# Performance work log

Measured on AMD Instinct MI355X. Metric: run time of the kernel, lower is better.

The kernel has to match this reference:

```python
import jax, jax.numpy as jnp
import numpy as np

V, B, C, H, W, D = 3, 2, 16, 128, 128, 32


def _skew(w):
    wx, wy, wz = w[..., 0], w[..., 1], w[..., 2]
    z = jnp.zeros_like(wx)
    return jnp.stack([
        jnp.stack([z, -wz, wy], -1),
        jnp.stack([wz, z, -wx], -1),
        jnp.stack([-wy, wx, z], -1)], -2)


def _rodrigues(w):
    th = jnp.linalg.norm(w, axis=-1, keepdims=True)
    n = w / (th + 1e-8)
    K = _skew(n)
    th = th[..., None]
    I = jnp.eye(3, dtype=w.dtype)
    return I + jnp.sin(th) * K + (1.0 - jnp.cos(th)) * (K @ K)


def setup_inputs() -> dict:
    key = jax.random.key(0)
    k1, k2, k3, k4 = jax.random.split(key, 4)
    features = jax.random.normal(k1, (V, B, C, H, W), jnp.float32)
    Kmat = jnp.array([[1.2 * W, 0.0, W / 2.0], [0.0, 1.2 * W, H / 2.0], [0.0, 0.0, 1.0]], jnp.float32)
    intrinsics = jnp.tile(Kmat, (V, B, 1, 1))
    rotvec = 0.05 * jax.random.normal(k2, (V, B, 3), jnp.float32)
    R = _rodrigues(rotvec)                                  # (V,B,3,3)
    t = 0.1 * jax.random.normal(k3, (V, B, 3), jnp.float32)
    top = jnp.concatenate([R, t[..., None]], -1)            # (V,B,3,4)
    bot = jnp.broadcast_to(jnp.array([0.0, 0.0, 0.0, 1.0], jnp.float32), (V, B, 1, 4))
    cam_to_world = jnp.concatenate([top, bot], -2)          # (V,B,4,4)
    depth_hypo = 1.0 + 9.0 * jax.random.uniform(k4, (B, D, H, W), jnp.float32)
    return {"features": features, "intrinsics": intrinsics,
            "cam_to_world": cam_to_world, "depth_hypo": depth_hypo}


def _grid_sample(img, grid):
    # img (B,C,H,W), grid (B,Hg,Wg,2) in [-1,1]; bilinear, zeros padding, align_corners=False
    Bb, Cc, Hh, Ww = img.shape
    gx = (grid[..., 0] + 1.0) * (Ww * 0.5) - 0.5
    gy = (grid[..., 1] + 1.0) * (Hh * 0.5) - 0.5
    x0f, y0f = jnp.floor(gx), jnp.floor(gy)
    fx, fy = gx - x0f, gy - y0f
    x0, y0 = x0f.astype(jnp.int32), y0f.astype(jnp.int32)

    def gather(xi, yi):
        valid = ((xi >= 0) & (xi < Ww) & (yi >= 0) & (yi < Hh)).astype(img.dtype)
        xc = jnp.clip(xi, 0, Ww - 1)
        yc = jnp.clip(yi, 0, Hh - 1)
        v = jax.vmap(lambda im, y, x: im[:, y, x])(img, yc, xc)  # (B,C,Hg,Wg)
        return v * valid[:, None]

    v00 = gather(x0, y0)
    v01 = gather(x0 + 1, y0)
    v10 = gather(x0, y0 + 1)
    v11 = gather(x0 + 1, y0 + 1)
    fx_, fy_ = fx[:, None], fy[:, None]
    return (v00 * (1 - fx_) * (1 - fy_) + v01 * fx_ * (1 - fy_)
            + v10 * (1 - fx_) * fy_ + v11 * fx_ * fy_)


def _unfold5(x):
    # x (B,K,H,W) -> (B,K,25,H,W); kernel 5, stride 1, pad 2; row-major kernel order (torch F.unfold)
    Hh, Ww = x.shape[-2], x.shape[-1]
    xp = jnp.pad(x, ((0, 0), (0, 0), (2, 2), (2, 2)))
    return jnp.stack([xp[..., i:i + Hh, j:j + Ww] for i in range(5) for j in range(5)], axis=2)


def _safe_norm(x, axis, keepdims=False):
    s = jnp.sum(x * x, axis=axis, keepdims=keepdims)
    z = s == 0
    return jnp.where(z, 0.0, jnp.sqrt(jnp.where(z, 1.0, s)))


def _homo_warp(src_f, depth_hypo, src_K, src_c2w, ref_K, ref_c2w):
    Bb, Cc, Hh, Ww = src_f.shape
    Dd = depth_hypo.shape[1]
    src_w2c = jnp.linalg.inv(src_c2w)
    ref_w2c = jnp.linalg.inv(ref_c2w)
    src_KK = src_w2c.at[:, :3, :3].set(src_K)
    ref_KK = ref_w2c.at[:, :3, :3].set(ref_K)
    proj = (src_KK @ src_w2c) @ jnp.linalg.inv(ref_KK @ ref_w2c)
    rot, trans = proj[:, :3, :3], proj[:, :3, 3:4]
    # NOTE: source uses arange(height) for both axes (square images assumed)
    ys, xs = jnp.meshgrid(jnp.arange(Hh, dtype=jnp.float32), jnp.arange(Hh, dtype=jnp.float32), indexing='ij')
    xyz = jnp.stack([xs.ravel(), ys.ravel(), jnp.ones(Hh * Ww, jnp.float32)], 0)  # (3,HW)
    rot_xyz = jnp.einsum('bij,jn->bin', rot, xyz)                                 # (B,3,HW)
    pts = rot_xyz[:, :, None, :] * depth_hypo.reshape(Bb, 1, Dd, -1) + trans[:, :, None, :]
    xy = pts[:, :2] / pts[:, 2:3]
    gx = xy[:, 0] / ((Ww - 1) / 2.0) - 1.0
    gy = xy[:, 1] / ((Hh - 1) / 2.0) - 1.0
    grid = jax.lax.stop_gradient(jnp.stack([gx, gy], -1).reshape(Bb, Dd * Hh, Ww, 2))
    return _grid_sample(src_f, grid).reshape(Bb, Cc, Dd, Hh, Ww)


def reference(features, intrinsics, cam_to_world, depth_hypo):
    Vv = features.shape[0]
    ref_f = features[0]
    warped = jnp.stack([
        _homo_warp(features[i], depth_hypo, intrinsics[i], cam_to_world[i],
                   intrinsics[0], cam_to_world[0]) for i in range(1, Vv)], 0)
    # faithful to in-place ref_volume.sub_: view k compares against ref - cumsum(warped[:k+1])
    diff = ref_f[None, :, :, None] - jnp.cumsum(warped, 0)        # (V-1,B,C,D,H,W)
    costs = _safe_norm(diff, axis=2)                              # (V-1,B,D,H,W)
    cost_volume = jnp.min(costs, axis=0)                          # (B,D,H,W)

    cnb = _unfold5(cost_volume)                                   # (B,D,25,H,W)
    dnb = _unfold5(depth_hypo)                                    # (B,D,25,H,W)
    w_depth = jax.nn.softmax(jnp.abs(dnb - dnb[:, :, 12:13]), axis=2)
    fnb = _unfold5(ref_f)                                         # (B,C,25,H,W)
    w_feat = _safe_norm(fnb - fnb[:, :, 12:13], axis=1, keepdims=True)  # (B,1,25,H,W)
    agg = jnp.sum(cnb * (w_depth * w_feat), axis=2)               # (B,D,H,W)

    prob = jax.nn.softmax(agg, axis=1)
    return jnp.sum(prob * depth_hypo, axis=1)                     # (B,H,W)
```

## Files before the change

kernel.cpp:

```cpp
#include <hip/hip_runtime.h>
#include <hip/hip_fp16.h>
#include <math.h>

#define Vn 3
#define Bn 2
#define Cn 16
#define Hn 128
#define Wn 128
#define Dn 32
#define HWn (Hn*Wn)
#define KD 4
#define PX 8

__device__ __forceinline__ void loadC8(float* r, const __half* p) {
    union { float4 f; __half2 h[4]; } u;
    u.f = *(const float4*)p;
    #pragma unroll
    for (int j = 0; j < 4; j++) {
        float2 a = __half22float2(u.h[j]);
        r[2*j] = a.x; r[2*j+1] = a.y;
    }
}

__global__ void transpose_kernel(const float* __restrict__ feat,
                                 __half* __restrict__ featH,
                                 const float* __restrict__ intr,
                                 const float* __restrict__ c2w,
                                 float* __restrict__ proj) {
    int idx = blockIdx.x * blockDim.x + threadIdx.x;
    if (idx < Vn * Bn * HWn) {
        int p  = idx % HWn;
        int vb = idx / HWn;
        const float* src = feat + (size_t)vb * Cn * HWn + p;
        union { float4 f[2]; __half h[16]; } u;
        #pragma unroll
        for (int c = 0; c < Cn; c++) u.h[c] = __float2half(src[(size_t)c * HWn]);
        float4* dst = (float4*)(featH + (size_t)idx * Cn);
        dst[0] = u.f[0];
        dst[1] = u.f[1];
    }

    if (blockIdx.x == 0 && threadIdx.x < (Vn - 1) * Bn) {
        int t  = threadIdx.x;
        int vi = t / Bn;
        int b  = t % Bn;
        int v  = vi + 1;

        const float* Ks = intr + (v * Bn + b) * 9;
        const float* Cs = c2w  + (v * Bn + b) * 16;
        const float* Kr = intr + (0 * Bn + b) * 9;
        const float* Cr = c2w  + (0 * Bn + b) * 16;

        float Ms[9], ms[3], Mr[9], mr[3];
        for (int which = 0; which < 2; which++) {
            const float* K = which ? Kr : Ks;
            const float* C = which ? Cr : Cs;
            float* M  = which ? Mr : Ms;
            float* mv = which ? mr : ms;
            float R[9], tt[3];
            for (int i = 0; i < 3; i++) {
                for (int j = 0; j < 3; j++) R[i*3+j] = C[i*4+j];
                tt[i] = C[i*4+3];
            }
            float tw[3];
            for (int i = 0; i < 3; i++)
                tw[i] = -(R[0*3+i]*tt[0] + R[1*3+i]*tt[1] + R[2*3+i]*tt[2]);
            for (int i = 0; i < 3; i++)
                for (int j = 0; j < 3; j++)
                    M[i*3+j] = K[i*3+0]*R[j*3+0] + K[i*3+1]*R[j*3+1] + K[i*3+2]*R[j*3+2];
            for (int i = 0; i < 3; i++)
                mv[i] = K[i*3+0]*tw[0] + K[i*3+1]*tw[1] + K[i*3+2]*tw[2] + tw[i];
        }

        float a = Mr[0], bb = Mr[1], c = Mr[2];
        float d = Mr[3], e  = Mr[4], f = Mr[5];
        float g = Mr[6], h  = Mr[7], i2 = Mr[8];
        float A_ = (e*i2 - f*h), B_ = (f*g - d*i2), C_ = (d*h - e*g);
        float det = a*A_ + bb*B_ + c*C_;
        float id = 1.0f / det;
        float inv[9];
        inv[0] = A_*id;            inv[1] = (c*h - bb*i2)*id;  inv[2] = (bb*f - c*e)*id;
        inv[3] = B_*id;            inv[4] = (a*i2 - c*g)*id;   inv[5] = (c*d - a*f)*id;
        inv[6] = C_*id;            inv[7] = (bb*g - a*h)*id;   inv[8] = (a*e - bb*d)*id;

        float rot[9], trans[3];
        for (int r = 0; r < 3; r++)
            for (int cc = 0; cc < 3; cc++)
                rot[r*3+cc] = Ms[r*3+0]*inv[0*3+cc] + Ms[r*3+1]*inv[1*3+cc] + Ms[r*3+2]*inv[2*3+cc];
        for (int r = 0; r < 3; r++)
            trans[r] = ms[r] - (rot[r*3+0]*mr[0] + rot[r*3+1]*mr[1] + rot[r*3+2]*mr[2]);

        float* o = proj + t * 12;
        for (int k = 0; k < 9; k++) o[k] = rot[k];
        for (int k = 0; k < 3; k++) o[9+k] = trans[k];
    }
}

__global__ void __launch_bounds__(256)
cost_kernel(const __half* __restrict__ featH,
            const float* __restrict__ depth,
            const float* __restrict__ proj,
            float* __restrict__ cv) {
    int idx = blockIdx.x * blockDim.x + threadIdx.x;
    if (idx >= Bn * (Dn/KD) * HWn) return;
    int x  = idx % Wn;
    int y  = (idx / Wn) % Hn;
    int dg = (idx / HWn) % (Dn/KD);
    int b  = idx / ((Dn/KD) * HWn);

    float dep[KD];
    #pragma unroll
    for (int i = 0; i < KD; i++)
        dep[i] = depth[(size_t)(b * Dn + dg*KD + i) * HWn + y * Wn + x];

    float s[KD][2];
    #pragma unroll
    for (int i = 0; i < KD; i++) { s[i][0] = 0.0f; s[i][1] = 0.0f; }

    const float fxp = (float)x, fyp = (float)y;
    const size_t pix0 = ((size_t)(0 * Bn + b) * HWn + y * Wn + x) * Cn;

    #pragma unroll
    for (int h = 0; h < 2; h++) {
        float ref8[8];
        loadC8(ref8, featH + pix0 + h * 8);

        float cum[KD][8];
        #pragma unroll
        for (int i = 0; i < KD; i++)
            #pragma unroll
            for (int j = 0; j < 8; j++) cum[i][j] = 0.0f;

        #pragma unroll
        for (int vi = 0; vi < Vn - 1; vi++) {
            const float* P = proj + (vi * Bn + b) * 12;
            float rx = P[0]*fxp + P[1]*fyp + P[2];
            float ry = P[3]*fxp + P[4]*fyp + P[5];
            float rz = P[6]*fxp + P[7]*fyp + P[8];
            const __half* sf = featH + (size_t)((vi + 1) * Bn + b) * HWn * Cn + h * 8;

            #pragma unroll
            for (int i = 0; i < KD; i++) {
                float px = rx * dep[i] + P[9];
                float py = ry * dep[i] + P[10];
                float pz = rz * dep[i] + P[11];
                float inz = 1.0f / pz;
                float sx = px * inz * ((float)Wn / (float)(Wn - 1)) - 0.5f;
                float sy = py * inz * ((float)Hn / (float)(Hn - 1)) - 0.5f;

                float x0f = floorf(sx), y0f = floorf(sy);
                float fx = sx - x0f, fy = sy - y0f;
                int x0 = (int)x0f, y0 = (int)y0f;
                int x1 = x0 + 1, y1 = y0 + 1;
                bool vx0 = (x0 >= 0) && (x0 < Wn);
                bool vx1 = (x1 >= 0) && (x1 < Wn);
                bool vy0 = (y0 >= 0) && (y0 < Hn);
                bool vy1 = (y1 >= 0) && (y1 < Hn);
                int xc0 = min(max(x0, 0), Wn - 1), xc1 = min(max(x1, 0), Wn - 1);
                int yc0 = min(max(y0, 0), Hn - 1), yc1 = min(max(y1, 0), Hn - 1);
                float m00 = (vx0 && vy0) ? (1.0f - fx) * (1.0f - fy) : 0.0f;
                float m01 = (vx1 && vy0) ? fx * (1.0f - fy) : 0.0f;
                float m10 = (vx0 && vy1) ? (1.0f - fx) * fy : 0.0f;
                float m11 = (vx1 && vy1) ? fx * fy : 0.0f;

                float t00[8], t01[8], t10[8], t11[8];
                loadC8(t00, sf + (size_t)(yc0 * Wn + xc0) * Cn);
                loadC8(t01, sf + (size_t)(yc0 * Wn + xc1) * Cn);
                loadC8(t10, sf + (size_t)(yc1 * Wn + xc0) * Cn);
                loadC8(t11, sf + (size_t)(yc1 * Wn + xc1) * Cn);

                float acc = 0.0f;
                #pragma unroll
                for (int j = 0; j < 8; j++) {
                    float val = m00 * t00[j] + m01 * t01[j] + m10 * t10[j] + m11 * t11[j];
                    cum[i][j] += val;
                    float df = ref8[j] - cum[i][j];
                    acc += df * df;
                }
                s[i][vi] += acc;
            }
        }
    }
    #pragma unroll
    for (int i = 0; i < KD; i++)
        cv[(size_t)(b * Dn + dg*KD + i) * HWn + y * Wn + x] =
            fminf(sqrtf(s[i][0]), sqrtf(s[i][1]));
}

__global__ void __launch_bounds__(256)
aggfinal_kernel(const float* __restrict__ cv,
                const float* __restrict__ depth,
                const __half* __restrict__ featH,
                float* __restrict__ out) {
    __shared__ float sd[Dn][5][PX + 4];
    __shared__ float sc[Dn][5][PX + 4];
    __shared__ float4 sfeatv[5][PX + 4][2];
    __shared__ float swf[25][PX];
    __shared__ float sagg[Dn][PX];

    int bi = blockIdx.x;
    int xt = bi % (Wn / PX);
    int y  = (bi / (Wn / PX)) % Hn;
    int b  = bi / (Hn * (Wn / PX));
    int x0 = xt * PX;
    int tid = threadIdx.x;

    const int NS = Dn * 5 * (PX + 4);
    for (int s = tid; s < NS; s += 256) {
        int d  = s / (5 * (PX + 4));
        int r  = s % (5 * (PX + 4));
        int ny = r / (PX + 4);
        int nx = r % (PX + 4);
        int gy = y - 2 + ny;
        int gx = x0 - 2 + nx;
        float dv = 0.0f, cvv = 0.0f;
        if (gy >= 0 && gy < Hn && gx >= 0 && gx < Wn) {
            size_t off = (size_t)(b * Dn + d) * HWn + gy * Wn + gx;
            dv  = depth[off];
            cvv = cv[off];
        }
        sd[d][ny][nx] = dv;
        sc[d][ny][nx] = cvv;
    }
    for (int s = tid; s < 5 * (PX + 4); s += 256) {
        int ny = s / (PX + 4);
        int nx = s % (PX + 4);
        int gy = y - 2 + ny;
        int gx = x0 - 2 + nx;
        if (gy >= 0 && gy < Hn && gx >= 0 && gx < Wn) {
            const float4* src = (const float4*)(featH +
                ((size_t)(0 * Bn + b) * HWn + gy * Wn + gx) * Cn);
            sfeatv[ny][nx][0] = src[0];
            sfeatv[ny][nx][1] = src[1];
        } else {
            float4 z = make_float4(0.f, 0.f, 0.f, 0.f);
            sfeatv[ny][nx][0] = z;
            sfeatv[ny][nx][1] = z;
        }
    }
    __syncthreads();

    for (int s = tid; s < 25 * PX; s += 256) {
        int k   = s / PX;
        int xi2 = s % PX;
        const __half2* ctrp = (const __half2*)&sfeatv[2][xi2 + 2][0];
        const __half2* nbp  = (const __half2*)&sfeatv[k / 5][xi2 + (k % 5)][0];
        float acc = 0.0f;
        #pragma unroll
        for (int j = 0; j < 8; j++) {
            float2 a = __half22float2(nbp[j]);
            float2 c = __half22float2(ctrp[j]);
            float dx0 = a.x - c.x, dy0 = a.y - c.y;
            acc += dx0 * dx0 + dy0 * dy0;
        }
        swf[k][xi2] = sqrtf(acc);
    }
    __syncthreads();

    int xi = tid % PX;
    int d  = tid / PX;

    float ctr = sd[d][2][xi + 2];
    float aarr[25];
    float mx = -3.402823e38f;
    #pragma unroll
    for (int k = 0; k < 25; k++) {
        float dn = sd[d][k / 5][xi + k % 5];
        aarr[k] = fabsf(dn - ctr);
        mx = fmaxf(mx, aarr[k]);
    }
    float den = 0.0f, num = 0.0f;
    #pragma unroll
    for (int k = 0; k < 25; k++) {
        float e = __expf(aarr[k] - mx);
        den += e;
        num += sc[d][k / 5][xi + k % 5] * e * swf[k][xi];
    }
    sagg[d][xi] = num / den;
    __syncthreads();

    if (tid < PX) {
        int p = tid;
        float m = -3.402823e38f;
        #pragma unroll
        for (int dd = 0; dd < Dn; dd++)
            m = fmaxf(m, sagg[dd][p]);
        float dn2 = 0.0f, nm2 = 0.0f;
        #pragma unroll
        for (int dd = 0; dd < Dn; dd++) {
            float e = __expf(sagg[dd][p] - m);
            dn2 += e;
            nm2 += e * sd[dd][2][p + 2];
        }
        out[(size_t)(b * Hn + y) * Wn + x0 + p] = nm2 / dn2;
    }
}

extern "C" void kernel_launch(void* const* d_in, const int* in_sizes, int n_in,
                              void* d_out, int out_size, void* d_ws, size_t ws_size,
                              hipStream_t stream) {
    const float* feat  = (const float*)d_in[0];
    const float* intr  = (const float*)d_in[1];
    const float* c2w   = (const float*)d_in[2];
    const float* depth = (const float*)d_in[3];
    float* out = (float*)d_out;

    float* ws    = (float*)d_ws;
    float* proj  = ws;
    __half* featH = (__half*)(ws + 64);
    float* cv    = ws + 64 + (Vn * Bn * HWn * Cn) / 2;

    int n_tr = Vn * Bn * HWn;
    transpose_kernel<<<(n_tr + 255) / 256, 256, 0, stream>>>(feat, featH, intr, c2w, proj);

    int n_cost = Bn * (Dn / KD) * HWn;
    cost_kernel<<<(n_cost + 255) / 256, 256, 0, stream>>>(featH, depth, proj, cv);

    int n_blk = Bn * Hn * (Wn / PX);
    aggfinal_kernel<<<n_blk, 256, 0, stream>>>(cv, depth, featH, out);
}
```

Before: 115.7 us.

## Reorder cost loop by depth-first channels and widen aggregation tile

Result: no change. 116.4 us (+0.5%).

```diff
diff --git a/kernel.cpp b/kernel.cpp
--- a/kernel.cpp
+++ b/kernel.cpp
@@ -10,7 +10,7 @@
 #define Dn 32
 #define HWn (Hn*Wn)
 #define KD 4
-#define PX 8
+#define PX 16
 
 __device__ __forceinline__ void loadC8(float* r, const __half* p) {
     union { float4 f; __half2 h[4]; } u;
@@ -113,78 +113,85 @@
     for (int i = 0; i < KD; i++)
         dep[i] = depth[(size_t)(b * Dn + dg*KD + i) * HWn + y * Wn + x];
 
-    float s[KD][2];
-    #pragma unroll
-    for (int i = 0; i < KD; i++) { s[i][0] = 0.0f; s[i][1] = 0.0f; }
+    float ref[Cn];
+    const size_t pix0 = ((size_t)(0 * Bn + b) * HWn + y * Wn + x) * Cn;
+    loadC8(ref,     featH + pix0);
+    loadC8(ref + 8, featH + pix0 + 8);
 
     const float fxp = (float)x, fyp = (float)y;
-    const size_t pix0 = ((size_t)(0 * Bn + b) * HWn + y * Wn + x) * Cn;
-
-    #pragma unroll
-    for (int h = 0; h < 2; h++) {
-        float ref8[8];
-        loadC8(ref8, featH + pix0 + h * 8);
-
-        float cum[KD][8];
-        #pragma unroll
-        for (int i = 0; i < KD; i++)
+
+    float rxv[2], ryv[2], rzv[2], txv[2], tyv[2], tzv[2];
+    #pragma unroll
+    for (int vi = 0; vi < Vn - 1; vi++) {
+        const float* P = proj + (vi * Bn + b) * 12;
+        rxv[vi] = P[0]*fxp + P[1]*fyp + P[2];
+        ryv[vi] = P[3]*fxp + P[4]*fyp + P[5];
+        rzv[vi] = P[6]*fxp + P[7]*fyp + P[8];
+        txv[vi] = P[9]; tyv[vi] = P[10]; tzv[vi] = P[11];
+    }
+    const __half* sfv[2] = {
+        featH + (size_t)(1 * Bn + b) * HWn * Cn,
+        featH + (size_t)(2 * Bn + b) * HWn * Cn
+    };
+
+    #pragma unroll
+    for (int i = 0; i < KD; i++) {
+        float cum[Cn];
+        #pragma unroll
+        for (int c = 0; c < Cn; c++) cum[c] = 0.0f;
+        float best = 3.402823e38f;
+
+        #pragma unroll
+        for (int vi = 0; vi < Vn - 1; vi++) {
+            float px = rxv[vi] * dep[i] + txv[vi];
+            float py = ryv[vi] * dep[i] + tyv[vi];
+            float pz = rzv[vi] * dep[i] + tzv[vi];
+            float inz = 1.0f / pz;
+            float sx = px * inz * ((float)Wn / (float)(Wn - 1)) - 0.5f;
+            float sy = py * inz * ((float)Hn / (float)(Hn - 1)) - 0.5f;
+
+            float x0f = floorf(sx), y0f = floorf(sy);
+            float fx = sx - x0f, fy = sy - y0f;
+            int x0 = (int)x0f, y0 = (int)y0f;
+            int x1 = x0 + 1, y1 = y0 + 1;
+            bool vx0 = (x0 >= 0) && (x0 < Wn);
+            bool vx1 = (x1 >= 0) && (x1 < Wn);
+            bool vy0 = (y0 >= 0) && (y0 < Hn);
+            bool vy1 = (y1 >= 0) && (y1 < Hn);
+            int xc0 = min(max(x0, 0), Wn - 1), xc1 = min(max(x1, 0), Wn - 1);
+            int yc0 = min(max(y0, 0), Hn - 1), yc1 = min(max(y1, 0), Hn - 1);
+            float m00 = (vx0 && vy0) ? (1.0f - fx) * (1.0f - fy) : 0.0f;
+            float m01 = (vx1 && vy0) ? fx * (1.0f - fy) : 0.0f;
+            float m10 = (vx0 && vy1) ? (1.0f - fx) * fy : 0.0f;
+            float m11 = (vx1 && vy1) ? fx * fy : 0.0f;
+
+            const __half* sf = sfv[vi];
+            size_t o00 = (size_t)(yc0 * Wn + xc0) * Cn;
+            size_t o01 = (size_t)(yc0 * Wn + xc1) * Cn;
+            size_t o10 = (size_t)(yc1 * Wn + xc0) * Cn;
+            size_t o11 = (size_t)(yc1 * Wn + xc1) * Cn;
+
+            float s = 0.0f;
             #pragma unroll
-            for (int j = 0; j < 8; j++) cum[i][j] = 0.0f;
-
-        #pragma unroll
-        for (int vi = 0; vi < Vn - 1; vi++) {
-            const float* P = proj + (vi * Bn + b) * 12;
-            float rx = P[0]*fxp + P[1]*fyp + P[2];
-            float ry = P[3]*fxp + P[4]*fyp + P[5];
-            float rz = P[6]*fxp + P[7]*fyp + P[8];
-            const __half* sf = featH + (size_t)((vi + 1) * Bn + b) * HWn * Cn + h * 8;
-
-            #pragma unroll
-            for (int i = 0; i < KD; i++) {
-                float px = rx * dep[i] + P[9];
-                float py = ry * dep[i] + P[10];
-                float pz = rz * dep[i] + P[11];
-                float inz = 1.0f / pz;
-                float sx = px * inz * ((float)Wn / (float)(Wn - 1)) - 0.5f;
-                float sy = py * inz * ((float)Hn / (float)(Hn - 1)) - 0.5f;
-
-                float x0f = floorf(sx), y0f = floorf(sy);
-                float fx = sx - x0f, fy = sy - y0f;
-                int x0 = (int)x0f, y0 = (int)y0f;
-                int x1 = x0 + 1, y1 = y0 + 1;
-                bool vx0 = (x0 >= 0) && (x0 < Wn);
-                bool vx1 = (x1 >= 0) && (x1 < Wn);
-                bool vy0 = (y0 >= 0) && (y0 < Hn);
-                bool vy1 = (y1 >= 0) && (y1 < Hn);
-                int xc0 = min(max(x0, 0), Wn - 1), xc1 = min(max(x1, 0), Wn - 1);
-                int yc0 = min(max(y0, 0), Hn - 1), yc1 = min(max(y1, 0), Hn - 1);
-                float m00 = (vx0 && vy0) ? (1.0f - fx) * (1.0f - fy) : 0.0f;
-                float m01 = (vx1 && vy0) ? fx * (1.0f - fy) : 0.0f;
-                float m10 = (vx0 && vy1) ? (1.0f - fx) * fy : 0.0f;
-                float m11 = (vx1 && vy1) ? fx * fy : 0.0f;
-
+            for (int h = 0; h < 2; h++) {
                 float t00[8], t01[8], t10[8], t11[8];
-                loadC8(t00, sf + (size_t)(yc0 * Wn + xc0) * Cn);
-                loadC8(t01, sf + (size_t)(yc0 * Wn + xc1) * Cn);
-                loadC8(t10, sf + (size_t)(yc1 * Wn + xc0) * Cn);
-                loadC8(t11, sf + (size_t)(yc1 * Wn + xc1) * Cn);
-
-                float acc = 0.0f;
+                loadC8(t00, sf + o00 + h * 8);
+                loadC8(t01, sf + o01 + h * 8);
+                loadC8(t10, sf + o10 + h * 8);
+                loadC8(t11, sf + o11 + h * 8);
                 #pragma unroll
                 for (int j = 0; j < 8; j++) {
+                    int c = h * 8 + j;
                     float val = m00 * t00[j] + m01 * t01[j] + m10 * t10[j] + m11 * t11[j];
-                    cum[i][j] += val;
-                    float df = ref8[j] - cum[i][j];
-                    acc += df * df;
+                    cum[c] += val;
+                    float df = ref[c] - cum[c];
+                    s += df * df;
                 }
-                s[i][vi] += acc;
             }
-        }
-    }
-    #pragma unroll
-    for (int i = 0; i < KD; i++)
-        cv[(size_t)(b * Dn + dg*KD + i) * HWn + y * Wn + x] =
-            fminf(sqrtf(s[i][0]), sqrtf(s[i][1]));
+            best = fminf(best, sqrtf(s));
+        }
+        cv[(size_t)(b * Dn + dg*KD + i) * HWn + y * Wn + x] = best;
+    }
 }
 
 __global__ void __launch_bounds__(256)
@@ -257,26 +264,30 @@
     }
     __syncthreads();
 
-    int xi = tid % PX;
-    int d  = tid / PX;
-
-    float ctr = sd[d][2][xi + 2];
-    float aarr[25];
-    float mx = -3.402823e38f;
-    #pragma unroll
-    for (int k = 0; k < 25; k++) {
-        float dn = sd[d][k / 5][xi + k % 5];
-        aarr[k] = fabsf(dn - ctr);
-        mx = fmaxf(mx, aarr[k]);
-    }
-    float den = 0.0f, num = 0.0f;
-    #pragma unroll
-    for (int k = 0; k < 25; k++) {
-        float e = __expf(aarr[k] - mx);
-        den += e;
-        num += sc[d][k / 5][xi + k % 5] * e * swf[k][xi];
-    }
-    sagg[d][xi] = num / den;
+    #pragma unroll
+    for (int q = 0; q < 2; q++) {
+        int task = tid + q * 256;
+        int xi = task % PX;
+        int d  = task / PX;
+
+        float ctr = sd[d][2][xi + 2];
+        float aarr[25];
+        float mx = -3.402823e38f;
+        #pragma unroll
+        for (int k = 0; k < 25; k++) {
+            float dn = sd[d][k / 5][xi + k % 5];
+            aarr[k] = fabsf(dn - ctr);
+            mx = fmaxf(mx, aarr[k]);
+        }
+        float den = 0.0f, num = 0.0f;
+        #pragma unroll
+        for (int k = 0; k < 25; k++) {
+            float e = __expf(aarr[k] - mx);
+            den += e;
+            num += sc[d][k / 5][xi + k % 5] * e * swf[k][xi];
+        }
+        sagg[d][xi] = num / den;
+    }
     __syncthreads();
 
     if (tid < PX) {
```
